# Kernel tuning notes

Measured on AMD Instinct MI355X. Metric: run time of the kernel, lower is better.

The kernel has to match this reference:

```python
import math
import jax, jax.numpy as jnp
import numpy as np

# --- model constants (from TECAN.__init__ defaults) ---
N = 180
DT = 0.02
SIGMA = 40.0
V_PREF = 22.0
RHO_DEG = 0.5
K = 0.0005
WR = 0.94
W_VS = 0.2
TAU = 1.0
RHO_W = 1.0 / RHO_DEG  # 2.0

B, T = 256, 1024


def _circ(a, b):
    return (a - b + 180.0) % 360.0 - 180.0


def setup_inputs() -> dict:
    key = jax.random.key(0)
    k_vel, k_bv, k_ro = jax.random.split(key, 3)

    xs = jnp.linspace(-180.0, 180.0 - 1.0 / RHO_DEG, N)
    coeff = WR / (math.sqrt(2 * math.pi) * SIGMA) * RHO_W
    gauss = lambda d: jnp.exp(-d ** 2 / (2 * SIGMA ** 2))
    W_r = coeff * gauss(_circ(xs[:, None], xs[None, :]))
    W_plus = coeff * gauss(_circ(xs[:, None], xs[None, :] + V_PREF))
    W_minus = coeff * gauss(_circ(xs[:, None], xs[None, :] - V_PREF))

    U_peak = WR * (1 + math.sqrt(1 - 0.896 ** 2 / WR ** 2)) / (4 * math.sqrt(math.pi) * K * SIGMA)
    u_s0 = U_peak * jnp.exp(-xs ** 2 / (4 * SIGMA ** 2))
    h_init = jnp.concatenate([u_s0, jnp.zeros_like(u_s0), jnp.zeros_like(u_s0)])  # [3N]

    vel = jax.random.normal(k_vel, (B, T, 1), dtype=jnp.float32)
    B_v = jax.random.normal(k_bv, (1,), dtype=jnp.float32) / 10.0
    # torch Linear(N,1,bias=False) init: U(-1/sqrt(N), 1/sqrt(N))
    readout_W = jax.random.uniform(k_ro, (1, N), dtype=jnp.float32,
                                   minval=-1.0 / math.sqrt(N), maxval=1.0 / math.sqrt(N))
    return {"vel": vel, "B_v": B_v, "readout_W": readout_W,
            "W_r": W_r, "W_plus": W_plus, "W_minus": W_minus, "h_init": h_init}


def _rates_s(u_s):
    up = jnp.maximum(u_s, 0.0)
    num = up ** 2
    return num / (1.0 + K * RHO_W * jnp.sum(num, axis=-1, keepdims=True))


def reference(vel, B_v, readout_W, W_r, W_plus, W_minus, h_init):
    n = W_r.shape[0]

    def step(h, v_t):
        # h: [B, 3N], v_t: [B, 1]
        u_s, u_p, u_m = h[:, :n], h[:, n:2 * n], h[:, 2 * n:]
        v = v_t * B_v  # [B,1]
        r_s = _rates_s(u_s)
        r_p = jnp.maximum((10.0 + v) * u_p, 0.0)
        r_m = jnp.maximum((10.0 - v) * u_m, 0.0)
        rec = r_s @ W_r.T + r_p @ W_plus.T + r_m @ W_minus.T
        du_s = (-u_s + RHO_W * rec) / TAU
        du_p = (-u_p + W_VS * r_s) / TAU
        du_m = (-u_m + W_VS * r_s) / TAU
        h_new = h + DT * jnp.concatenate([du_s, du_p, du_m], axis=-1)
        out_t = _rates_s(h_new[:, :n]) @ readout_W.T  # [B,1]
        return h_new, out_t

    h0 = jnp.broadcast_to(h_init[None, :], (vel.shape[0], h_init.shape[0]))
    vel_t = jnp.swapaxes(vel, 0, 1)  # [T,B,1]
    _, outs = jax.lax.scan(step, h0, vel_t)  # outs: [T,B,1]
    return jnp.swapaxes(outs, 0, 1)  # [B,T,1]
```

## Files before the change

### kernel.cpp

```cpp
#include <hip/hip_runtime.h>
#include <math.h>

#define NN 180
#define TSTEPS 1024

typedef float v2f __attribute__((ext_vector_type(2)));
__device__ __forceinline__ v2f bc(float s) { v2f r; r.x = s; r.y = s; return r; }
__device__ __forceinline__ v2f mk2(float a, float b) { v2f r; r.x = a; r.y = b; return r; }
__device__ __forceinline__ v2f pkfma(v2f a, v2f b, v2f c) { return __builtin_elementwise_fma(a, b, c); }

template<int CTRL>
__device__ __forceinline__ float dpp_add_b(float x) {
    int y = __builtin_amdgcn_update_dpp(0, __builtin_bit_cast(int, x),
                                        CTRL, 0xF, 0xF, true);
    return x + __builtin_bit_cast(float, y);
}
__device__ __forceinline__ float rl63(float x) {
    return __builtin_bit_cast(float,
        __builtin_amdgcn_readlane(__builtin_bit_cast(int, x), 63));
}
__device__ __forceinline__ float wsum64(float x) {
    x = dpp_add_b<0xB1>(x); x = dpp_add_b<0x4E>(x); x = dpp_add_b<0x141>(x);
    x = dpp_add_b<0x140>(x); x = dpp_add_b<0x142>(x); x = dpp_add_b<0x143>(x);
    return rl63(x);
}

__global__ __launch_bounds__(64, 1) void ring_sim(
    const float* __restrict__ vel,
    const float* __restrict__ B_v,
    const float* __restrict__ ro_w,
    const float* __restrict__ W_r,
    const float* __restrict__ h_init,
    float* __restrict__ out)
{
    const int b = blockIdx.x;
    const int l = threadIdx.x;

    __shared__ float lds_v8[TSTEPS];
    __shared__ v2f   zh[4 * TSTEPS + 4 * 64];

    {
        const float s = B_v[0] * 0.008f;
        for (int i = l; i < TSTEPS; i += 64)
            lds_v8[i] = vel[b * TSTEPS + i] * s;
    }

    float us0[3], w0[3], ro3[3], kk[3];
    int   dj[3];
    #pragma unroll
    for (int c = 0; c < 3; ++c) {
        int d = l + 64 * c;
        bool okc = (d < NN);
        dj[c]  = okc ? d : 0;
        us0[c] = okc ? h_init[d]              : 0.f;
        w0[c]  = okc ? h_init[NN + d] * 250.f : 0.f;
        ro3[c] = okc ? ro_w[d]                : 0.f;
        kk[c]  = okc ? W_r[d * NN]            : 0.f;
    }

    float Ra[7], Rb[7];
    float a_[4], bb[4], Wa[4], Wb[4], g[4];
    #pragma unroll
    for (int n = 0; n < 7; ++n) {
        float sc = 0.f, ss = 0.f, sk = 0.f, uc = 0.f, usn = 0.f, wc = 0.f, wsn = 0.f;
        #pragma unroll
        for (int c = 0; c < 3; ++c) {
            float ang = 0.0349065850398865915f * (float)((n * dj[c]) % NN);
            float cn = cosf(ang), sn = sinf(ang);
            sc = fmaf(ro3[c], cn, sc);  ss = fmaf(ro3[c], sn, ss);
            if (n < 4) {
                sk  = fmaf(kk[c],  cn, sk);
                uc  = fmaf(us0[c], cn, uc);  usn = fmaf(us0[c], sn, usn);
                wc  = fmaf(w0[c],  cn, wc);  wsn = fmaf(w0[c],  sn, wsn);
            }
        }
        Ra[n] = ((n == 0) ? 1.f : 2.f) * wsum64(sc);
        Rb[n] = 2.f * wsum64(ss);
        if (n < 4) {
            g[n]  = 0.04f * wsum64(sk);
            a_[n] = wsum64(uc)  * (1.f / 180.f);
            bb[n] = wsum64(usn) * (1.f / 180.f);
            Wa[n] = wsum64(wc)  * (1.f / 180.f);
            Wb[n] = wsum64(wsn) * (1.f / 180.f);
        }
    }

    const float w11 = 0.38397243543875251f;
    const float C110 = 0.08f;
    const float C111 = 0.08f * cosf(w11),       s111 = sinf(w11);
    const float C112 = 0.08f * cosf(2.f * w11), s112 = sinf(2.f * w11);
    const float C113 = 0.08f * cosf(3.f * w11), s113 = sinf(3.f * w11);

    float a0 = a_[0];
    v2f z1 = mk2(a_[1], bb[1]), z2 = mk2(a_[2], bb[2]), z3 = mk2(a_[3], bb[3]);
    float W0 = Wa[0];
    v2f W1 = mk2(0.5f * Wa[1], 0.5f * Wb[1]);
    v2f W2 = mk2(0.5f * Wa[2], 0.5f * Wb[2]);
    v2f W3 = mk2(0.5f * Wa[3], 0.5f * Wb[3]);
    const float g0 = g[0];
    const float gg1 = 2.f * g[1], gg2 = 2.f * g[2], gg3 = 2.f * g[3];

    const int zbase = (l == 0) ? 0 : (4 * TSTEPS + 4 * l);

    __builtin_amdgcn_wave_barrier();

    float v_use = lds_v8[0];

    #pragma unroll 2
    for (int t = 0; t < TSTEPS; ++t) {
        v2f s = z1 * z1; s = pkfma(z2, z2, s); s = pkfma(z3, z3, s);
        const float d0 = fmaf(a0, a0, 2.f * (s.x + s.y));

        v2f d1 = bc(a0) * z1;
        d1 = pkfma(bc(z1.x), z2, d1);
        d1 = pkfma(mk2(z1.y, -z1.y), mk2(z2.y, z2.x), d1);
        d1 = pkfma(bc(z2.x), z3, d1);
        d1 = pkfma(mk2(z2.y, -z2.y), mk2(z3.y, z3.x), d1);

        v2f d2 = bc(a0) * z2;
        d2 = pkfma(bc(z1.x), z3, d2);
        d2 = pkfma(mk2(z1.y, -z1.y), mk2(z3.y, z3.x), d2);
        const float hx = 0.5f * z1.x, hy = 0.5f * z1.y;
        d2 = pkfma(bc(hx), z1, d2);
        d2 = pkfma(mk2(-hy, hy), mk2(z1.y, z1.x), d2);

        v2f d3 = bc(a0) * z3;
        d3 = pkfma(bc(z1.x), z2, d3);
        d3 = pkfma(mk2(-z1.y, z1.y), mk2(z2.y, z2.x), d3);

        const float inv = __builtin_amdgcn_rcpf(fmaf(d0, 0.18f, 1.0f));
        const float rs0 = inv * d0;
        v2f r1 = bc(inv) * d1, r2 = bc(inv) * d2, r3 = bc(inv) * d3;

        const float v = v_use;
        v_use = lds_v8[(t + 1) & (TSTEPS - 1)];
        const float t1 = v * s111, t2 = v * s112, t3 = v * s113;

        float q0 = fmaf(C110, W0, rs0);
        v2f q1 = pkfma(bc(C111), W1, r1); q1 = pkfma(bc(t1), mk2(-W1.y, W1.x), q1);
        v2f q2 = pkfma(bc(C112), W2, r2); q2 = pkfma(bc(t2), mk2(-W2.y, W2.x), q2);
        v2f q3 = pkfma(bc(C113), W3, r3); q3 = pkfma(bc(t3), mk2(-W3.y, W3.x), q3);

        W0 = fmaf(0.98f, W0, rs0);
        W1 = pkfma(bc(0.98f), W1, r1);
        W2 = pkfma(bc(0.98f), W2, r2);
        W3 = pkfma(bc(0.98f), W3, r3);

        a0 = fmaf(0.98f, a0, g0 * q0);
        z1 = pkfma(bc(0.98f), z1, bc(gg1) * q1);
        z2 = pkfma(bc(0.98f), z2, bc(gg2) * q2);
        z3 = pkfma(bc(0.98f), z3, bc(gg3) * q3);

        const int zi = zbase + ((l == 0) ? 4 * t : 0);
        zh[zi + 0] = z1;
        zh[zi + 1] = z2;
        zh[zi + 2] = z3;
        zh[zi + 3] = mk2(a0, 0.f);
    }

    __builtin_amdgcn_wave_barrier();

    #pragma unroll
    for (int k = 0; k < TSTEPS / 64; ++k) {
        const int t = 64 * k + l;
        v2f Z1 = zh[4 * t + 0], Z2 = zh[4 * t + 1], Z3 = zh[4 * t + 2];
        const float A0 = zh[4 * t + 3].x;
        const float A1 = Z1.x, B1 = Z1.y, A2 = Z2.x, B2 = Z2.y, A3 = Z3.x, B3 = Z3.y;

        float n2 = A1 * A1; n2 = fmaf(B1, B1, n2); n2 = fmaf(A2, A2, n2);
        n2 = fmaf(B2, B2, n2); n2 = fmaf(A3, A3, n2); n2 = fmaf(B3, B3, n2);
        float D0 = fmaf(A0, A0, 2.f * n2);
        float p1 = A0 * A1; p1 = fmaf(A1, A2, p1); p1 = fmaf(B1, B2, p1);
        p1 = fmaf(A2, A3, p1); p1 = fmaf(B2, B3, p1);
        float D1 = 2.f * p1;
        float p2 = A0 * A2; p2 = fmaf(A1, A3, p2); p2 = fmaf(B1, B3, p2);
        float D2 = fmaf(A1, A1, fmaf(-B1, B1, 2.f * p2));
        float p3 = A1 * A2; p3 = fmaf(-B1, B2, p3); p3 = fmaf(A0, A3, p3);
        float D3 = 2.f * p3;
        float p4 = A1 * A3; p4 = fmaf(-B1, B3, p4);
        float D4 = fmaf(A2, A2, fmaf(-B2, B2, 2.f * p4));
        float p5 = A2 * A3; p5 = fmaf(-B2, B3, p5);
        float D5 = 2.f * p5;
        float D6 = fmaf(A3, A3, -(B3 * B3));
        float q1 = A0 * B1; q1 = fmaf(A1, B2, q1); q1 = fmaf(-A2, B1, q1);
        q1 = fmaf(A2, B3, q1); q1 = fmaf(-A3, B2, q1);
        float e1 = 2.f * q1;
        float q2_ = A1 * B1; q2_ = fmaf(A0, B2, q2_); q2_ = fmaf(A1, B3, q2_);
        q2_ = fmaf(-A3, B1, q2_);
        float e2 = 2.f * q2_;
        float q3 = A1 * B2; q3 = fmaf(A2, B1, q3); q3 = fmaf(A0, B3, q3);
        float e3 = 2.f * q3;
        float q4 = A2 * B2; q4 = fmaf(A1, B3, q4); q4 = fmaf(A3, B1, q4);
        float e4 = 2.f * q4;
        float q5 = A2 * B3; q5 = fmaf(A3, B2, q5);
        float e5 = 2.f * q5;
        float e6 = 2.f * (A3 * B3);

        const float inv = __builtin_amdgcn_rcpf(fmaf(D0, 0.18f, 1.0f));
        float dq = D0 * Ra[0];
        dq = fmaf(D1, Ra[1], dq); dq = fmaf(e1, Rb[1], dq);
        dq = fmaf(D2, Ra[2], dq); dq = fmaf(e2, Rb[2], dq);
        dq = fmaf(D3, Ra[3], dq); dq = fmaf(e3, Rb[3], dq);
        dq = fmaf(D4, Ra[4], dq); dq = fmaf(e4, Rb[4], dq);
        dq = fmaf(D5, Ra[5], dq); dq = fmaf(e5, Rb[5], dq);
        dq = fmaf(D6, Ra[6], dq); dq = fmaf(e6, Rb[6], dq);

        out[b * TSTEPS + t] = dq * inv;
    }
}

extern "C" void kernel_launch(void* const* d_in, const int* in_sizes, int n_in,
                              void* d_out, int out_size, void* d_ws, size_t ws_size,
                              hipStream_t stream) {
    const float* vel    = (const float*)d_in[0];
    const float* B_v    = (const float*)d_in[1];
    const float* ro_w   = (const float*)d_in[2];
    const float* W_r    = (const float*)d_in[3];
    const float* h_init = (const float*)d_in[6];

    const int B = in_sizes[0] / TSTEPS;
    ring_sim<<<dim3(B), dim3(64), 0, stream>>>(vel, B_v, ro_w, W_r, h_init, (float*)d_out);
}
```

Before: 168.4 us.

## Pack two batch elements per wave using packed-math lanes in recurrence

Each wave now simulates two batch sequences at once, with the x and y halves of packed float2 math holding the two independent recurrences instead of the real and imaginary parts of one. The grid is halved, velocity is streamed from global memory as float4 prefetches rather than staged in LDS, and the v*B_v scale is folded into constants. The history layout is reshaped so the readout phase processes 32 timesteps for each of the two sequences per pass. This trades more serial work per wave for full use of the packed FMA width and fewer waves, which can lose parallelism since only 128 blocks run.

```diff
diff --git a/kernel.cpp b/kernel.cpp
--- a/kernel.cpp
+++ b/kernel.cpp
@@ -3,6 +3,7 @@
 
 #define NN 180
 #define TSTEPS 1024
+#define HSTRIDE 14
 
 typedef float v2f __attribute__((ext_vector_type(2)));
 __device__ __forceinline__ v2f bc(float s) { v2f r; r.x = s; r.y = s; return r; }
@@ -25,7 +26,7 @@
     return rl63(x);
 }
 
-__global__ __launch_bounds__(64, 1) void ring_sim(
+__global__ __launch_bounds__(64, 1) void ring_duo(
     const float* __restrict__ vel,
     const float* __restrict__ B_v,
     const float* __restrict__ ro_w,
@@ -36,14 +37,8 @@
     const int b = blockIdx.x;
     const int l = threadIdx.x;
 
-    __shared__ float lds_v8[TSTEPS];
-    __shared__ v2f   zh[4 * TSTEPS + 4 * 64];
-
-    {
-        const float s = B_v[0] * 0.008f;
-        for (int i = l; i < TSTEPS; i += 64)
-            lds_v8[i] = vel[b * TSTEPS + i] * s;
-    }
+    __shared__ float hist[HSTRIDE * TSTEPS];
+    __shared__ float dump[HSTRIDE * 64];
 
     float us0[3], w0[3], ro3[3], kk[3];
     int   dj[3];
@@ -58,8 +53,7 @@
         kk[c]  = okc ? W_r[d * NN]            : 0.f;
     }
 
-    float Ra[7], Rb[7];
-    float a_[4], bb[4], Wa[4], Wb[4], g[4];
+    float Ra[7], Rb[7], a_[4], bb[4], Wa[4], Wb[4], g[4];
     #pragma unroll
     for (int n = 0; n < 7; ++n) {
         float sc = 0.f, ss = 0.f, sk = 0.f, uc = 0.f, usn = 0.f, wc = 0.f, wsn = 0.f;
@@ -86,86 +80,111 @@
     }
 
     const float w11 = 0.38397243543875251f;
-    const float C110 = 0.08f;
-    const float C111 = 0.08f * cosf(w11),       s111 = sinf(w11);
-    const float C112 = 0.08f * cosf(2.f * w11), s112 = sinf(2.f * w11);
-    const float C113 = 0.08f * cosf(3.f * w11), s113 = sinf(3.f * w11);
-
-    float a0 = a_[0];
-    v2f z1 = mk2(a_[1], bb[1]), z2 = mk2(a_[2], bb[2]), z3 = mk2(a_[3], bb[3]);
-    float W0 = Wa[0];
-    v2f W1 = mk2(0.5f * Wa[1], 0.5f * Wb[1]);
-    v2f W2 = mk2(0.5f * Wa[2], 0.5f * Wb[2]);
-    v2f W3 = mk2(0.5f * Wa[3], 0.5f * Wb[3]);
-    const float g0 = g[0];
-    const float gg1 = 2.f * g[1], gg2 = 2.f * g[2], gg3 = 2.f * g[3];
-
-    const int zbase = (l == 0) ? 0 : (4 * TSTEPS + 4 * l);
+    const float vs  = B_v[0] * 0.008f;
+    const v2f C0 = bc(0.08f);
+    const v2f C1 = bc(0.08f * cosf(w11)),       svs1 = bc(vs * sinf(w11));
+    const v2f C2 = bc(0.08f * cosf(2.f * w11)), svs2 = bc(vs * sinf(2.f * w11));
+    const v2f C3 = bc(0.08f * cosf(3.f * w11)), svs3 = bc(vs * sinf(3.f * w11));
+    const v2f gd0 = bc(g[0]);
+    const v2f gd1 = bc(2.f * g[1]), gd2 = bc(2.f * g[2]), gd3 = bc(2.f * g[3]);
+    const v2f p98 = bc(0.98f), halfv = bc(0.5f), c018 = bc(0.18f), onev = bc(1.f);
+
+    v2f a0  = bc(a_[0]);
+    v2f zr1 = bc(a_[1]), zi1 = bc(bb[1]);
+    v2f zr2 = bc(a_[2]), zi2 = bc(bb[2]);
+    v2f zr3 = bc(a_[3]), zi3 = bc(bb[3]);
+    v2f W0  = bc(g[0] * Wa[0]);
+    v2f W1x = bc(g[1] * Wa[1]), W1y = bc(g[1] * Wb[1]);
+    v2f W2x = bc(g[2] * Wa[2]), W2y = bc(g[2] * Wb[2]);
+    v2f W3x = bc(g[3] * Wa[3]), W3y = bc(g[3] * Wb[3]);
+
+    float* hp = (l == 0) ? hist : (dump + HSTRIDE * l);
+    const int hstep = (l == 0) ? HSTRIDE : 0;
+
+    const float4* vpA = (const float4*)(vel + (size_t)(2 * b)     * TSTEPS);
+    const float4* vpB = (const float4*)(vel + (size_t)(2 * b + 1) * TSTEPS);
+
+    auto step = [&](v2f vd) {
+        v2f s = zr1 * zr1; s = pkfma(zi1, zi1, s); s = pkfma(zr2, zr2, s);
+        s = pkfma(zi2, zi2, s); s = pkfma(zr3, zr3, s); s = pkfma(zi3, zi3, s);
+        const v2f d0 = pkfma(a0, a0, s + s);
+
+        v2f p1 = a0 * zr1; p1 = pkfma(zr1, zr2, p1); p1 = pkfma(zi1, zi2, p1);
+        p1 = pkfma(zr2, zr3, p1); p1 = pkfma(zi2, zi3, p1);
+        v2f q1 = a0 * zi1; q1 = pkfma(zr1, zi2, q1); q1 = pkfma(-zr2, zi1, q1);
+        q1 = pkfma(zr2, zi3, q1); q1 = pkfma(-zr3, zi2, q1);
+        v2f P1 = zr1 * zr1; P1 = pkfma(-zi1, zi1, P1);
+        v2f p2 = a0 * zr2; p2 = pkfma(zr1, zr3, p2); p2 = pkfma(zi1, zi3, p2);
+        const v2f d2r = pkfma(halfv, P1, p2);
+        v2f q2 = zr1 * zi1; q2 = pkfma(a0, zi2, q2); q2 = pkfma(zr1, zi3, q2);
+        q2 = pkfma(-zr3, zi1, q2);
+        v2f p3 = zr1 * zr2; p3 = pkfma(-zi1, zi2, p3); p3 = pkfma(a0, zr3, p3);
+        v2f q3 = zr1 * zi2; q3 = pkfma(zr2, zi1, q3); q3 = pkfma(a0, zi3, q3);
+
+        const v2f x = pkfma(d0, c018, onev);
+        v2f inv;
+        inv.x = __builtin_amdgcn_rcpf(x.x);
+        inv.y = __builtin_amdgcn_rcpf(x.y);
+
+        const v2f gv0 = gd0 * inv, gv1 = gd1 * inv, gv2 = gd2 * inv, gv3 = gd3 * inv;
+        const v2f gr0 = gv0 * d0;
+        const v2f g1x = gv1 * p1,  g1y = gv1 * q1;
+        const v2f g2x = gv2 * d2r, g2y = gv2 * q2;
+        const v2f g3x = gv3 * p3,  g3y = gv3 * q3;
+        const v2f t1 = svs1 * vd, t2 = svs2 * vd, t3 = svs3 * vd;
+
+        const v2f u0 = pkfma(C0, W0, gr0);
+        v2f u1x = pkfma(C1, W1x, g1x); u1x = pkfma(-t1, W1y, u1x);
+        v2f u1y = pkfma(C1, W1y, g1y); u1y = pkfma( t1, W1x, u1y);
+        v2f u2x = pkfma(C2, W2x, g2x); u2x = pkfma(-t2, W2y, u2x);
+        v2f u2y = pkfma(C2, W2y, g2y); u2y = pkfma( t2, W2x, u2y);
+        v2f u3x = pkfma(C3, W3x, g3x); u3x = pkfma(-t3, W3y, u3x);
+        v2f u3y = pkfma(C3, W3y, g3y); u3y = pkfma( t3, W3x, u3y);
+
+        W0  = pkfma(p98, W0,  gr0);
+        W1x = pkfma(p98, W1x, g1x); W1y = pkfma(p98, W1y, g1y);
+        W2x = pkfma(p98, W2x, g2x); W2y = pkfma(p98, W2y, g2y);
+        W3x = pkfma(p98, W3x, g3x); W3y = pkfma(p98, W3y, g3y);
+
+        a0  = pkfma(p98, a0,  u0);
+        zr1 = pkfma(p98, zr1, u1x); zi1 = pkfma(p98, zi1, u1y);
+        zr2 = pkfma(p98, zr2, u2x); zi2 = pkfma(p98, zi2, u2y);
+        zr3 = pkfma(p98, zr3, u3x); zi3 = pkfma(p98, zi3, u3y);
+    };
+
+    float4 vA = vpA[0], vB = vpB[0];
+    step(mk2(vA.x, vB.x));
+
+    #pragma unroll 1
+    for (int blk = 0; blk < TSTEPS / 4; ++blk) {
+        const float4 vnA = (blk < TSTEPS / 4 - 1) ? vpA[blk + 1] : vA;
+        const float4 vnB = (blk < TSTEPS / 4 - 1) ? vpB[blk + 1] : vB;
+        #pragma unroll
+        for (int c = 0; c < 4; ++c) {
+            v2f* hv = (v2f*)hp;
+            hv[0] = a0;  hv[1] = zr1; hv[2] = zi1;
+            hv[3] = zr2; hv[4] = zi2; hv[5] = zr3; hv[6] = zi3;
+            hp += hstep;
+            const v2f vv = (c == 0) ? mk2(vA.y, vB.y)
+                         : (c == 1) ? mk2(vA.z, vB.z)
+                         : (c == 2) ? mk2(vA.w, vB.w)
+                         :            mk2(vnA.x, vnB.x);
+            step(vv);
+        }
+        vA = vnA; vB = vnB;
+    }
 
     __builtin_amdgcn_wave_barrier();
 
-    float v_use = lds_v8[0];
-
-    #pragma unroll 2
-    for (int t = 0; t < TSTEPS; ++t) {
-        v2f s = z1 * z1; s = pkfma(z2, z2, s); s = pkfma(z3, z3, s);
-        const float d0 = fmaf(a0, a0, 2.f * (s.x + s.y));
-
-        v2f d1 = bc(a0) * z1;
-        d1 = pkfma(bc(z1.x), z2, d1);
-        d1 = pkfma(mk2(z1.y, -z1.y), mk2(z2.y, z2.x), d1);
-        d1 = pkfma(bc(z2.x), z3, d1);
-        d1 = pkfma(mk2(z2.y, -z2.y), mk2(z3.y, z3.x), d1);
-
-        v2f d2 = bc(a0) * z2;
-        d2 = pkfma(bc(z1.x), z3, d2);
-        d2 = pkfma(mk2(z1.y, -z1.y), mk2(z3.y, z3.x), d2);
-        const float hx = 0.5f * z1.x, hy = 0.5f * z1.y;
-        d2 = pkfma(bc(hx), z1, d2);
-        d2 = pkfma(mk2(-hy, hy), mk2(z1.y, z1.x), d2);
-
-        v2f d3 = bc(a0) * z3;
-        d3 = pkfma(bc(z1.x), z2, d3);
-        d3 = pkfma(mk2(-z1.y, z1.y), mk2(z2.y, z2.x), d3);
-
-        const float inv = __builtin_amdgcn_rcpf(fmaf(d0, 0.18f, 1.0f));
-        const float rs0 = inv * d0;
-        v2f r1 = bc(inv) * d1, r2 = bc(inv) * d2, r3 = bc(inv) * d3;
-
-        const float v = v_use;
-        v_use = lds_v8[(t + 1) & (TSTEPS - 1)];
-        const float t1 = v * s111, t2 = v * s112, t3 = v * s113;
-
-        float q0 = fmaf(C110, W0, rs0);
-        v2f q1 = pkfma(bc(C111), W1, r1); q1 = pkfma(bc(t1), mk2(-W1.y, W1.x), q1);
-        v2f q2 = pkfma(bc(C112), W2, r2); q2 = pkfma(bc(t2), mk2(-W2.y, W2.x), q2);
-        v2f q3 = pkfma(bc(C113), W3, r3); q3 = pkfma(bc(t3), mk2(-W3.y, W3.x), q3);
-
-        W0 = fmaf(0.98f, W0, rs0);
-        W1 = pkfma(bc(0.98f), W1, r1);
-        W2 = pkfma(bc(0.98f), W2, r2);
-        W3 = pkfma(bc(0.98f), W3, r3);
-
-        a0 = fmaf(0.98f, a0, g0 * q0);
-        z1 = pkfma(bc(0.98f), z1, bc(gg1) * q1);
-        z2 = pkfma(bc(0.98f), z2, bc(gg2) * q2);
-        z3 = pkfma(bc(0.98f), z3, bc(gg3) * q3);
-
-        const int zi = zbase + ((l == 0) ? 4 * t : 0);
-        zh[zi + 0] = z1;
-        zh[zi + 1] = z2;
-        zh[zi + 2] = z3;
-        zh[zi + 3] = mk2(a0, 0.f);
-    }
-
-    __builtin_amdgcn_wave_barrier();
-
-    #pragma unroll
-    for (int k = 0; k < TSTEPS / 64; ++k) {
-        const int t = 64 * k + l;
-        v2f Z1 = zh[4 * t + 0], Z2 = zh[4 * t + 1], Z3 = zh[4 * t + 2];
-        const float A0 = zh[4 * t + 3].x;
-        const float A1 = Z1.x, B1 = Z1.y, A2 = Z2.x, B2 = Z2.y, A3 = Z3.x, B3 = Z3.y;
+    const int s_ = l >> 5, tt = l & 31;
+    #pragma unroll 1
+    for (int it = 0; it < TSTEPS / 32; ++it) {
+        const int t = it * 32 + tt;
+        const float* hb = hist + HSTRIDE * t + s_;
+        const float A0 = hb[0];
+        const float A1 = hb[2],  B1 = hb[4];
+        const float A2 = hb[6],  B2 = hb[8];
+        const float A3 = hb[10], B3 = hb[12];
 
         float n2 = A1 * A1; n2 = fmaf(B1, B1, n2); n2 = fmaf(A2, A2, n2);
         n2 = fmaf(B2, B2, n2); n2 = fmaf(A3, A3, n2); n2 = fmaf(B3, B3, n2);
@@ -205,7 +224,7 @@
         dq = fmaf(D5, Ra[5], dq); dq = fmaf(e5, Rb[5], dq);
         dq = fmaf(D6, Ra[6], dq); dq = fmaf(e6, Rb[6], dq);
 
-        out[b * TSTEPS + t] = dq * inv;
+        out[(size_t)(2 * b + s_) * TSTEPS + t] = dq * inv;
     }
 }
 
@@ -219,5 +238,6 @@
     const float* h_init = (const float*)d_in[6];
 
     const int B = in_sizes[0] / TSTEPS;
-    ring_sim<<<dim3(B), dim3(64), 0, stream>>>(vel, B_v, ro_w, W_r, h_init, (float*)d_out);
-}
+    ring_duo<<<dim3(B / 2), dim3(64), 0, stream>>>(
+        vel, B_v, ro_w, W_r, h_init, (float*)d_out);
+}
```

After: 239.1 us. 42.0% more time.
